# Performance work log

Hardware: AMD Instinct MI355X
Metric: run time of the kernel (lower is better)

Reference implementation:

```python
import jax, jax.numpy as jnp
import numpy as np

D_MODEL = 512
N = 2048
BS = 8


def setup_inputs() -> dict:
    key = jax.random.key(0)
    ks = jax.random.split(key, 5)
    inputs1 = jax.random.normal(ks[0], (BS, N, D_MODEL), dtype=jnp.float32)
    inputs2 = jax.random.normal(ks[1], (BS, N, D_MODEL), dtype=jnp.float32)
    # torch Linear weights: init.normal_(std=0.001), bias=0
    Wq = 0.001 * jax.random.normal(ks[2], (D_MODEL, D_MODEL), dtype=jnp.float32)
    Wk = 0.001 * jax.random.normal(ks[3], (D_MODEL, D_MODEL), dtype=jnp.float32)
    Wv = 0.001 * jax.random.normal(ks[4], (D_MODEL, D_MODEL), dtype=jnp.float32)
    bq = jnp.zeros((D_MODEL,), dtype=jnp.float32)
    bk = jnp.zeros((D_MODEL,), dtype=jnp.float32)
    bv = jnp.zeros((D_MODEL,), dtype=jnp.float32)
    # nn.Parameter(torch.ones((n, n)))
    position_biases = jnp.ones((N, N), dtype=jnp.float32)
    return {"inputs1": inputs1, "inputs2": inputs2, "Wq": Wq, "bq": bq,
            "Wk": Wk, "bk": bk, "Wv": Wv, "bv": bv,
            "position_biases": position_biases}


def reference(inputs1, inputs2, Wq, bq, Wk, bk, Wv, bv, position_biases):
    # torch Linear: y = x @ W.T + b
    q = inputs1 @ Wq.T + bq                     # [b, n, d]
    k = inputs1 @ Wk.T + bk                     # [b, s, d]
    v = inputs2 @ Wv.T + bv                     # [b, s, d]
    # exp(k[b,s,d] + bias[t,s]) = exp(bias)[t,s] * exp(k)[b,s,d] -> separable,
    # avoiding the original's (n, bs, n, dim) broadcast intermediate.
    expB = jnp.exp(position_biases)             # [t, s]
    ek = jnp.exp(k)                             # [b, s, d]
    num = jnp.einsum('ts,bsd->btd', expB, ek * v)
    den = jnp.einsum('ts,bsd->btd', expB, ek)
    return jax.nn.sigmoid(q) * (num / den)      # [b, n, d]
```

## Files before the change

kernel.cpp:

```cpp
#include <hip/hip_runtime.h>

typedef float  f32x4  __attribute__((ext_vector_type(4)));
typedef __bf16 bf16x8 __attribute__((ext_vector_type(8)));
typedef __bf16 bf16x4 __attribute__((ext_vector_type(4)));

#define D_MODEL 512
#define SEQ     2048
#define BATCH   8
#define ROWS    (BATCH * SEQ)

#define ASYNC_COPY16(dst_lds, src_glb)                                          \
  __builtin_amdgcn_global_load_lds(                                             \
      (const __attribute__((address_space(1))) void*)(src_glb),                 \
      (__attribute__((address_space(3))) void*)(dst_lds), 16, 0, 0)

__global__ void cvt_all_kernel(const float* __restrict__ x1,
                               const float* __restrict__ x2,
                               const float* __restrict__ posb,
                               const float* __restrict__ Wq,
                               const float* __restrict__ Wk,
                               const float* __restrict__ Wv,
                               __bf16* __restrict__ x1b, __bf16* __restrict__ x2b,
                               __bf16* __restrict__ expBb, __bf16* __restrict__ wb)
{
  const int blk = blockIdx.x;
  if (blk < 16384) {
    const float* in = (blk < 8192) ? x1 : x2;
    __bf16* out = (blk < 8192) ? x1b : x2b;
    const int i = (blk & 8191) * 256 + threadIdx.x;
    float4 v = ((const float4*)in)[i];
    bf16x4 o = { (__bf16)v.x, (__bf16)v.y, (__bf16)v.z, (__bf16)v.w };
    ((bf16x4*)out)[i] = o;
  } else if (blk < 20480) {
    const int i = (blk - 16384) * 256 + threadIdx.x;
    float4 v = ((const float4*)posb)[i];
    bf16x4 o = { (__bf16)__expf(v.x), (__bf16)__expf(v.y),
                 (__bf16)__expf(v.z), (__bf16)__expf(v.w) };
    ((bf16x4*)expBb)[i] = o;
  } else {
    const int i = (blk - 20480) * 256 + threadIdx.x;
    const int nW4 = D_MODEL * D_MODEL / 4;
    const float* src = (i < nW4) ? Wq : (i < 2 * nW4) ? Wk : Wv;
    const int ii = i - ((i < nW4) ? 0 : (i < 2 * nW4) ? nW4 : 2 * nW4);
    float4 v = ((const float4*)src)[ii];
    bf16x4 o = { (__bf16)v.x, (__bf16)v.y, (__bf16)v.z, (__bf16)v.w };
    ((bf16x4*)wb)[i] = o;
  }
}

__global__ __launch_bounds__(512) void q_gemm_kernel(
    const __bf16* __restrict__ x1b, const __bf16* __restrict__ wb,
    const float* __restrict__ bq, __bf16* __restrict__ sigq)
{
  extern __shared__ __align__(16) __bf16 smem[];

  const int K = D_MODEL;
  const int tid  = threadIdx.x;
  const int wave = tid >> 6;
  const int lane = tid & 63;
  const int quad = lane >> 4;
  const int l16  = lane & 15;
  const int wm   = (wave >> 1) * 64;
  const int wn   = (wave & 1) * 64;
  const int m0   = blockIdx.x * 256;
  const int n0   = blockIdx.y * 128;
  const int l8r  = lane >> 3;
  const int scol = ((lane & 7) ^ l8r) * 8;

  const __bf16* ga[4]; const __bf16* gb[2];
  #pragma unroll
  for (int i = 0; i < 4; ++i)
    ga[i] = x1b + (long long)(m0 + i * 64 + wave * 8 + l8r) * K + scol;
  #pragma unroll
  for (int i = 0; i < 2; ++i)
    gb[i] = wb + (long long)(n0 + i * 64 + wave * 8 + l8r) * K + scol;

  f32x4 acc[4][4];
  #pragma unroll
  for (int i = 0; i < 4; ++i)
    #pragma unroll
    for (int j = 0; j < 4; ++j) acc[i][j] = (f32x4){0.f, 0.f, 0.f, 0.f};

  auto stageA2 = [&](int c, int k0, int i0) {
    ASYNC_COPY16(smem + c * 16384 + (i0 * 64 + wave * 8) * 64, ga[i0] + k0);
    ASYNC_COPY16(smem + c * 16384 + ((i0 + 1) * 64 + wave * 8) * 64, ga[i0 + 1] + k0);
  };
  auto stageB1 = [&](int c, int k0, int i) {
    ASYNC_COPY16(smem + 32768 + c * 8192 + (i * 64 + wave * 8) * 64, gb[i] + k0);
  };

  stageA2(0, 0, 0); stageA2(0, 0, 2);
  stageB1(0, 0, 0); stageB1(0, 0, 1);

  const int s0 = ((quad    ) ^ (l16 & 7)) * 8;
  const int s1 = ((quad + 4) ^ (l16 & 7)) * 8;

  for (int t = 0; t < 8; ++t) {
    const int c = t & 1;
    asm volatile("s_waitcnt vmcnt(0)" ::: "memory");
    __builtin_amdgcn_s_barrier();
    __builtin_amdgcn_sched_barrier(0);

    const __bf16* Ac = smem +         c * 16384 + (wm + l16) * 64;
    const __bf16* Bc = smem + 32768 + c * 8192  + (wn + l16) * 64;
    const bool pf = (t + 1 < 8);
    const int k1 = (t + 1) * 64;

    bf16x8 bfr[4][2];
    #pragma unroll
    for (int p = 0; p < 2; ++p) {
      if (p == 0) {
        #pragma unroll
        for (int j = 0; j < 4; ++j) {
          bfr[j][0] = *(const bf16x8*)&Bc[j * 1024 + s0];
          bfr[j][1] = *(const bf16x8*)&Bc[j * 1024 + s1];
        }
      }
      bf16x8 af[2][2];
      #pragma unroll
      for (int ii = 0; ii < 2; ++ii) {
        af[ii][0] = *(const bf16x8*)&Ac[(p * 2 + ii) * 1024 + s0];
        af[ii][1] = *(const bf16x8*)&Ac[(p * 2 + ii) * 1024 + s1];
      }
      if (pf) {
        if (p == 0) { stageA2(c ^ 1, k1, 0); stageB1(c ^ 1, k1, 0); }
        else        { stageA2(c ^ 1, k1, 2); stageB1(c ^ 1, k1, 1); }
      }
      __builtin_amdgcn_s_barrier();
      asm volatile("s_waitcnt lgkmcnt(0)" ::: "memory");
      __builtin_amdgcn_sched_barrier(0);
      __builtin_amdgcn_s_setprio(1);
      #pragma unroll
      for (int kk = 0; kk < 2; ++kk)
        #pragma unroll
        for (int ii = 0; ii < 2; ++ii)
          #pragma unroll
          for (int j = 0; j < 4; ++j)
            acc[p * 2 + ii][j] = __builtin_amdgcn_mfma_f32_16x16x32_bf16(
                af[ii][kk], bfr[j][kk], acc[p * 2 + ii][j], 0, 0, 0);
      __builtin_amdgcn_s_setprio(0);
      __builtin_amdgcn_s_barrier();
    }
  }

  #pragma unroll
  for (int j = 0; j < 4; ++j) {
    const int col = n0 + wn + j * 16 + l16;
    const float bvv = bq[col];
    #pragma unroll
    for (int i = 0; i < 4; ++i) {
      #pragma unroll
      for (int r = 0; r < 4; ++r) {
        const int row = m0 + wm + i * 16 + quad * 4 + r;
        float x = acc[i][j][r] + bvv;
        sigq[(long long)row * D_MODEL + col] = (__bf16)(1.f / (1.f + __expf(-x)));
      }
    }
  }
}

__global__ __launch_bounds__(512) void kv_fused_kernel(
    const __bf16* __restrict__ x1b, const __bf16* __restrict__ x2b,
    const __bf16* __restrict__ wb,
    const float* __restrict__ bk, const float* __restrict__ bv,
    __bf16* __restrict__ ekvT)
{
  extern __shared__ __align__(16) __bf16 smem[];

  const int K = D_MODEL;
  const int tid  = threadIdx.x;
  const int wave = tid >> 6;
  const int lane = tid & 63;
  const int quad = lane >> 4;
  const int l16  = lane & 15;
  const int wm   = (wave >> 1) * 64;
  const int wn   = (wave & 1) * 64;
  const int F0   = blockIdx.y * 256;
  const int L0   = blockIdx.x * 128;
  const int l8r  = lane >> 3;
  const int scol = ((lane & 7) ^ l8r) * 8;

  const __bf16* Wkb = wb + (long long)D_MODEL * D_MODEL;
  const __bf16* Wvb = wb + 2LL * D_MODEL * D_MODEL;

  const __bf16* gWk[4]; const __bf16* gWv[4];
  const __bf16* gX1[2]; const __bf16* gX2[2];
  #pragma unroll
  for (int i = 0; i < 4; ++i) {
    gWk[i] = Wkb + (long long)(F0 + i * 64 + wave * 8 + l8r) * K + scol;
    gWv[i] = Wvb + (long long)(F0 + i * 64 + wave * 8 + l8r) * K + scol;
  }
  #pragma unroll
  for (int i = 0; i < 2; ++i) {
    gX1[i] = x1b + (long long)(L0 + i * 64 + wave * 8 + l8r) * K + scol;
    gX2[i] = x2b + (long long)(L0 + i * 64 + wave * 8 + l8r) * K + scol;
  }

  f32x4 acck[4][4], accv[4][4];
  #pragma unroll
  for (int i = 0; i < 4; ++i)
    #pragma unroll
    for (int j = 0; j < 4; ++j) {
      acck[i][j] = (f32x4){0.f, 0.f, 0.f, 0.f};
      accv[i][j] = (f32x4){0.f, 0.f, 0.f, 0.f};
    }

  auto stgW = [&](int c, int i, const __bf16* p) {
    ASYNC_COPY16(smem + c * 16384 + (i * 64 + wave * 8) * 64, p);
  };
  auto stgX = [&](int c, int i, const __bf16* p) {
    ASYNC_COPY16(smem + 32768 + c * 8192 + (i * 64 + wave * 8) * 64, p);
  };

  stgW(0, 0, gWk[0]); stgW(0, 1, gWk[1]); stgW(0, 2, gWk[2]); stgW(0, 3, gWk[3]);
  stgX(0, 0, gX1[0]); stgX(0, 1, gX1[1]);

  const int s0 = ((quad    ) ^ (l16 & 7)) * 8;
  const int s1 = ((quad + 4) ^ (l16 & 7)) * 8;

  auto pass = [&](f32x4 (&acc)[4][4], bool vpass) {
    for (int t = 0; t < 8; ++t) {
      const int c = t & 1;
      asm volatile("s_waitcnt vmcnt(0)" ::: "memory");
      __builtin_amdgcn_s_barrier();
      __builtin_amdgcn_sched_barrier(0);

      const __bf16* Ac = smem +         c * 16384 + (wm + l16) * 64;
      const __bf16* Bc = smem + 32768 + c * 8192  + (wn + l16) * 64;
      const bool nx = (t == 7);
      const bool pf = !(vpass && nx);
      const bool sv = vpass || nx;
      const int k1 = nx ? 0 : (t + 1) * 64;

      bf16x8 bfr[4][2];
      #pragma unroll
      for (int p = 0; p < 2; ++p) {
        if (p == 0) {
          #pragma unroll
          for (int j = 0; j < 4; ++j) {
            bfr[j][0] = *(const bf16x8*)&Bc[j * 1024 + s0];
            bfr[j][1] = *(const bf16x8*)&Bc[j * 1024 + s1];
          }
        }
        bf16x8 af[2][2];
        #pragma unroll
        for (int ii = 0; ii < 2; ++ii) {
          af[ii][0] = *(const bf16x8*)&Ac[(p * 2 + ii) * 1024 + s0];
          af[ii][1] = *(const bf16x8*)&Ac[(p * 2 + ii) * 1024 + s1];
        }
        if (pf) {
          if (p == 0) {
            stgW(c ^ 1, 0, (sv ? gWv[0] : gWk[0]) + k1);
            stgW(c ^ 1, 1, (sv ? gWv[1] : gWk[1]) + k1);
            stgX(c ^ 1, 0, (sv ? gX2[0] : gX1[0]) + k1);
          } else {
            stgW(c ^ 1, 2, (sv ? gWv[2] : gWk[2]) + k1);
            stgW(c ^ 1, 3, (sv ? gWv[3] : gWk[3]) + k1);
            stgX(c ^ 1, 1, (sv ? gX2[1] : gX1[1]) + k1);
          }
        }
        __builtin_amdgcn_s_barrier();
        asm volatile("s_waitcnt lgkmcnt(0)" ::: "memory");
        __builtin_amdgcn_sched_barrier(0);
        __builtin_amdgcn_s_setprio(1);
        #pragma unroll
        for (int kk = 0; kk < 2; ++kk)
          #pragma unroll
          for (int ii = 0; ii < 2; ++ii)
            #pragma unroll
            for (int j = 0; j < 4; ++j)
              acc[p * 2 + ii][j] = __builtin_amdgcn_mfma_f32_16x16x32_bf16(
                  af[ii][kk], bfr[j][kk], acc[p * 2 + ii][j], 0, 0, 0);
        __builtin_amdgcn_s_setprio(0);
        __builtin_amdgcn_s_barrier();
      }
    }
  };

  pass(acck, false);
  pass(accv, true);

  const int b   = L0 >> 11;
  const int sb  = L0 & 2047;
  __bf16* outb = ekvT + (long long)b * (2 * D_MODEL) * SEQ + sb;
  #pragma unroll
  for (int i = 0; i < 4; ++i) {
    #pragma unroll
    for (int r = 0; r < 4; ++r) {
      const int d = F0 + wm + i * 16 + quad * 4 + r;
      const float bkd = bk[d];
      const float bvd = bv[d];
      const int gr = ((d >> 5) << 6) + (d & 31);
      #pragma unroll
      for (int j = 0; j < 4; ++j) {
        const int ss = wn + j * 16 + l16;
        const float kkv = acck[i][j][r] + bkd;
        const float vvv = accv[i][j][r] + bvd;
        const float ekf = __expf(kkv);
        outb[(long long)gr * SEQ + ss]        = (__bf16)(ekf * vvv);
        outb[(long long)(gr + 32) * SEQ + ss] = (__bf16)ekf;
      }
    }
  }
}

#define EBM 256
#define EBN 256
#define EBK 64
#define ENT (SEQ / EBK)

__global__ __launch_bounds__(512) void einsum_fused_kernel(
    const __bf16* __restrict__ A, const __bf16* __restrict__ BtAll,
    const __bf16* __restrict__ sigq, float* __restrict__ out)
{
  extern __shared__ __align__(16) __bf16 smem[];

  const int b = blockIdx.z;
  const __bf16* Bt = BtAll + (long long)b * (2 * D_MODEL) * SEQ;

  const int tid  = threadIdx.x;
  const int wave = tid >> 6;
  const int lane = tid & 63;
  const int quad = lane >> 4;
  const int l16  = lane & 15;
  const int wm   = (wave >> 2) * 128;
  const int wn   = (wave & 3) * 64;
  const int m0   = blockIdx.x * EBM;
  const int n0   = blockIdx.y * EBN;
  const int l8r  = lane >> 3;
  const int scol = ((lane & 7) ^ l8r) * 8;

  const __bf16* gA = A  + (long long)(m0 + wave * 8 + l8r) * SEQ + scol;
  const __bf16* gB = Bt + (long long)(n0 + wave * 8 + l8r) * SEQ + scol;
  __bf16* lA = smem +         (wave * 8) * 64;
  __bf16* lB = smem + 32768 + (wave * 8) * 64;

  f32x4 acc[8][4];
  #pragma unroll
  for (int i = 0; i < 8; ++i)
    #pragma unroll
    for (int j = 0; j < 4; ++j) acc[i][j] = (f32x4){0.f, 0.f, 0.f, 0.f};

  auto stage_pair = [&](int c, int k0, int i) {
    ASYNC_COPY16(lA + c * 16384 + i * 4096, gA + (long long)i * 64 * SEQ + k0);
    ASYNC_COPY16(lB + c * 16384 + i * 4096, gB + (long long)i * 64 * SEQ + k0);
  };

  #pragma unroll
  for (int i = 0; i < 4; ++i) stage_pair(0, 0, i);

  const int s0 = ((quad    ) ^ (l16 & 7)) * 8;
  const int s1 = ((quad + 4) ^ (l16 & 7)) * 8;

  for (int t = 0; t < ENT; ++t) {
    const int c = t & 1;
    asm volatile("s_waitcnt vmcnt(0)" ::: "memory");
    __builtin_amdgcn_s_barrier();
    __builtin_amdgcn_sched_barrier(0);

    const __bf16* Ac = smem +         c * 16384 + (wm + l16) * 64;
    const __bf16* Bc = smem + 32768 + c * 16384 + (wn + l16) * 64;
    const bool pf = (t + 1 < ENT);
    const int k1 = (t + 1) * EBK;

    bf16x8 bfr[4][2];
    #pragma unroll
    for (int q = 0; q < 4; ++q) {
      if (q == 0) {
        #pragma unroll
        for (int j = 0; j < 4; ++j) {
          bfr[j][0] = *(const bf16x8*)&Bc[j * 1024 + s0];
          bfr[j][1] = *(const bf16x8*)&Bc[j * 1024 + s1];
        }
      }
      bf16x8 af[2][2];
      #pragma unroll
      for (int ii = 0; ii < 2; ++ii) {
        af[ii][0] = *(const bf16x8*)&Ac[(q * 2 + ii) * 1024 + s0];
        af[ii][1] = *(const bf16x8*)&Ac[(q * 2 + ii) * 1024 + s1];
      }
      if (pf) {
        if (q == 0) { stage_pair(c ^ 1, k1, 0); stage_pair(c ^ 1, k1, 1); }
        else if (q == 1) { stage_pair(c ^ 1, k1, 2); stage_pair(c ^ 1, k1, 3); }
      }
      __builtin_amdgcn_s_barrier();
      asm volatile("s_waitcnt lgkmcnt(0)" ::: "memory");
      __builtin_amdgcn_sched_barrier(0);
      __builtin_amdgcn_s_setprio(1);
      #pragma unroll
      for (int kk = 0; kk < 2; ++kk)
        #pragma unroll
        for (int ii = 0; ii < 2; ++ii)
          #pragma unroll
          for (int j = 0; j < 4; ++j)
            acc[q * 2 + ii][j] = __builtin_amdgcn_mfma_f32_16x16x32_bf16(
                af[ii][kk], bfr[j][kk], acc[q * 2 + ii][j], 0, 0, 0);
      __builtin_amdgcn_s_setprio(0);
      __builtin_amdgcn_s_barrier();
    }
  }

  const int g = (n0 + wn) >> 6;
  #pragma unroll
  for (int j = 0; j < 2; ++j) {
    const int d = g * 32 + j * 16 + l16;
    #pragma unroll
    for (int i = 0; i < 8; ++i) {
      #pragma unroll
      for (int r = 0; r < 4; ++r) {
        const int row = m0 + wm + i * 16 + quad * 4 + r;
        const long long off = ((long long)b * SEQ + row) * D_MODEL + d;
        const float num = acc[i][j][r];
        const float den = acc[i][j + 2][r];
        out[off] = (float)sigq[off] * (num / den);
      }
    }
  }
}

extern "C" void kernel_launch(void* const* d_in, const int* in_sizes, int n_in,
                              void* d_out, int out_size, void* d_ws, size_t ws_size,
                              hipStream_t stream) {
  const float* inputs1 = (const float*)d_in[0];
  const float* inputs2 = (const float*)d_in[1];
  const float* Wq = (const float*)d_in[2];
  const float* bq = (const float*)d_in[3];
  const float* Wk = (const float*)d_in[4];
  const float* bk = (const float*)d_in[5];
  const float* Wv = (const float*)d_in[6];
  const float* bv = (const float*)d_in[7];
  const float* posb = (const float*)d_in[8];
  float* out = (float*)d_out;

  char* ws = (char*)d_ws;
  const long long szX  = (long long)ROWS * D_MODEL * 2;
  const long long szW  = (long long)D_MODEL * D_MODEL * 2;
  const long long szEB = (long long)SEQ * SEQ * 2;
  const long long szT  = (long long)BATCH * 2 * D_MODEL * SEQ * 2;
  __bf16* x1b   = (__bf16*)(ws);                 ws += szX;
  __bf16* x2b   = (__bf16*)(ws);                 ws += szX;
  __bf16* wb    = (__bf16*)(ws);                 ws += 3 * szW;
  __bf16* expBb = (__bf16*)(ws);                 ws += szEB;
  __bf16* sigq  = (__bf16*)(ws);                 ws += szX;
  __bf16* ekvT  = (__bf16*)(ws);                 ws += szT;

  static bool attr_done = false;
  if (!attr_done) {
    hipFuncSetAttribute((const void*)einsum_fused_kernel,
                        hipFuncAttributeMaxDynamicSharedMemorySize, 131072);
    hipFuncSetAttribute((const void*)q_gemm_kernel,
                        hipFuncAttributeMaxDynamicSharedMemorySize, 98304);
    hipFuncSetAttribute((const void*)kv_fused_kernel,
                        hipFuncAttributeMaxDynamicSharedMemorySize, 98304);
    attr_done = true;
  }

  cvt_all_kernel<<<21248, 256, 0, stream>>>(inputs1, inputs2, posb,
                                            Wq, Wk, Wv,
                                            x1b, x2b, expBb, wb);

  {
    dim3 g(ROWS / 256, D_MODEL / 128);
    q_gemm_kernel<<<g, 512, 98304, stream>>>(x1b, wb, bq, sigq);
  }

  {
    dim3 g(ROWS / 128, D_MODEL / 256);
    kv_fused_kernel<<<g, 512, 98304, stream>>>(x1b, x2b, wb, bk, bv, ekvT);
  }

  {
    dim3 g(SEQ / EBM, (2 * D_MODEL) / EBN, BATCH);
    einsum_fused_kernel<<<g, 512, 131072, stream>>>(expBb, ekvT, sigq, out);
  }
}
```

Baseline: 239.5 us.

## Fuse fp32-to-bf16 activation conversion into GEMM loaders

Drops the separate pass that converted both activation tensors to bf16. The Q and KV GEMMs now load fp32 activations straight into registers, convert them, and write bf16 into LDS in the swizzled layout. This removes a full write and re-read of two 16 MB bf16 buffers plus the work of many conversion blocks. In exchange, the GEMMs read twice as many activation bytes, the x1 tile is read and converted by both GEMMs, and the async LDS copy becomes a register round-trip with an extra lgkmcnt wait before each barrier.

New measurement: 246.8 us. 3.1% more time.

```diff
diff --git a/kernel.cpp b/kernel.cpp
--- a/kernel.cpp
+++ b/kernel.cpp
@@ -14,31 +14,28 @@
       (const __attribute__((address_space(1))) void*)(src_glb),                 \
       (__attribute__((address_space(3))) void*)(dst_lds), 16, 0, 0)
 
-__global__ void cvt_all_kernel(const float* __restrict__ x1,
-                               const float* __restrict__ x2,
-                               const float* __restrict__ posb,
+__device__ __forceinline__ bf16x8 cvt_f32x8(float4 a, float4 b) {
+  bf16x8 o;
+  o[0] = (__bf16)a.x; o[1] = (__bf16)a.y; o[2] = (__bf16)a.z; o[3] = (__bf16)a.w;
+  o[4] = (__bf16)b.x; o[5] = (__bf16)b.y; o[6] = (__bf16)b.z; o[7] = (__bf16)b.w;
+  return o;
+}
+
+__global__ void cvt_all_kernel(const float* __restrict__ posb,
                                const float* __restrict__ Wq,
                                const float* __restrict__ Wk,
                                const float* __restrict__ Wv,
-                               __bf16* __restrict__ x1b, __bf16* __restrict__ x2b,
                                __bf16* __restrict__ expBb, __bf16* __restrict__ wb)
 {
   const int blk = blockIdx.x;
-  if (blk < 16384) {
-    const float* in = (blk < 8192) ? x1 : x2;
-    __bf16* out = (blk < 8192) ? x1b : x2b;
-    const int i = (blk & 8191) * 256 + threadIdx.x;
-    float4 v = ((const float4*)in)[i];
-    bf16x4 o = { (__bf16)v.x, (__bf16)v.y, (__bf16)v.z, (__bf16)v.w };
-    ((bf16x4*)out)[i] = o;
-  } else if (blk < 20480) {
-    const int i = (blk - 16384) * 256 + threadIdx.x;
+  if (blk < 4096) {
+    const int i = blk * 256 + threadIdx.x;
     float4 v = ((const float4*)posb)[i];
     bf16x4 o = { (__bf16)__expf(v.x), (__bf16)__expf(v.y),
                  (__bf16)__expf(v.z), (__bf16)__expf(v.w) };
     ((bf16x4*)expBb)[i] = o;
   } else {
-    const int i = (blk - 20480) * 256 + threadIdx.x;
+    const int i = (blk - 4096) * 256 + threadIdx.x;
     const int nW4 = D_MODEL * D_MODEL / 4;
     const float* src = (i < nW4) ? Wq : (i < 2 * nW4) ? Wk : Wv;
     const int ii = i - ((i < nW4) ? 0 : (i < 2 * nW4) ? nW4 : 2 * nW4);
@@ -49,7 +46,7 @@
 }
 
 __global__ __launch_bounds__(512) void q_gemm_kernel(
-    const __bf16* __restrict__ x1b, const __bf16* __restrict__ wb,
+    const float* __restrict__ x1f, const __bf16* __restrict__ wb,
     const float* __restrict__ bq, __bf16* __restrict__ sigq)
 {
   extern __shared__ __align__(16) __bf16 smem[];
@@ -67,10 +64,10 @@
   const int l8r  = lane >> 3;
   const int scol = ((lane & 7) ^ l8r) * 8;
 
-  const __bf16* ga[4]; const __bf16* gb[2];
+  const float* gaf[4]; const __bf16* gb[2];
   #pragma unroll
   for (int i = 0; i < 4; ++i)
-    ga[i] = x1b + (long long)(m0 + i * 64 + wave * 8 + l8r) * K + scol;
+    gaf[i] = x1f + (long long)(m0 + i * 64 + wave * 8 + l8r) * K + scol;
   #pragma unroll
   for (int i = 0; i < 2; ++i)
     gb[i] = wb + (long long)(n0 + i * 64 + wave * 8 + l8r) * K + scol;
@@ -81,15 +78,22 @@
     #pragma unroll
     for (int j = 0; j < 4; ++j) acc[i][j] = (f32x4){0.f, 0.f, 0.f, 0.f};
 
-  auto stageA2 = [&](int c, int k0, int i0) {
-    ASYNC_COPY16(smem + c * 16384 + (i0 * 64 + wave * 8) * 64, ga[i0] + k0);
-    ASYNC_COPY16(smem + c * 16384 + ((i0 + 1) * 64 + wave * 8) * 64, ga[i0 + 1] + k0);
+  float4 aA[4][2];
+  auto loadA = [&](int k0, int i) {
+    aA[i][0] = *(const float4*)(gaf[i] + k0);
+    aA[i][1] = *(const float4*)(gaf[i] + k0 + 4);
+  };
+  auto writeA = [&](int c) {
+    #pragma unroll
+    for (int i = 0; i < 4; ++i)
+      *(bf16x8*)(smem + c * 16384 + (i * 64 + wave * 8) * 64 + lane * 8) =
+          cvt_f32x8(aA[i][0], aA[i][1]);
   };
   auto stageB1 = [&](int c, int k0, int i) {
     ASYNC_COPY16(smem + 32768 + c * 8192 + (i * 64 + wave * 8) * 64, gb[i] + k0);
   };
 
-  stageA2(0, 0, 0); stageA2(0, 0, 2);
+  loadA(0, 0); loadA(0, 1); loadA(0, 2); loadA(0, 3);
   stageB1(0, 0, 0); stageB1(0, 0, 1);
 
   const int s0 = ((quad    ) ^ (l16 & 7)) * 8;
@@ -98,6 +102,8 @@
   for (int t = 0; t < 8; ++t) {
     const int c = t & 1;
     asm volatile("s_waitcnt vmcnt(0)" ::: "memory");
+    writeA(c);
+    asm volatile("s_waitcnt lgkmcnt(0)" ::: "memory");
     __builtin_amdgcn_s_barrier();
     __builtin_amdgcn_sched_barrier(0);
 
@@ -123,8 +129,8 @@
         af[ii][1] = *(const bf16x8*)&Ac[(p * 2 + ii) * 1024 + s1];
       }
       if (pf) {
-        if (p == 0) { stageA2(c ^ 1, k1, 0); stageB1(c ^ 1, k1, 0); }
-        else        { stageA2(c ^ 1, k1, 2); stageB1(c ^ 1, k1, 1); }
+        if (p == 0) { loadA(k1, 0); loadA(k1, 1); stageB1(c ^ 1, k1, 0); }
+        else        { loadA(k1, 2); loadA(k1, 3); stageB1(c ^ 1, k1, 1); }
       }
       __builtin_amdgcn_s_barrier();
       asm volatile("s_waitcnt lgkmcnt(0)" ::: "memory");
@@ -160,7 +166,7 @@
 }
 
 __global__ __launch_bounds__(512) void kv_fused_kernel(
-    const __bf16* __restrict__ x1b, const __bf16* __restrict__ x2b,
+    const float* __restrict__ x1f, const float* __restrict__ x2f,
     const __bf16* __restrict__ wb,
     const float* __restrict__ bk, const float* __restrict__ bv,
     __bf16* __restrict__ ekvT)
@@ -184,7 +190,7 @@
   const __bf16* Wvb = wb + 2LL * D_MODEL * D_MODEL;
 
   const __bf16* gWk[4]; const __bf16* gWv[4];
-  const __bf16* gX1[2]; const __bf16* gX2[2];
+  const float*  gX1[2]; const float*  gX2[2];
   #pragma unroll
   for (int i = 0; i < 4; ++i) {
     gWk[i] = Wkb + (long long)(F0 + i * 64 + wave * 8 + l8r) * K + scol;
@@ -192,8 +198,8 @@
   }
   #pragma unroll
   for (int i = 0; i < 2; ++i) {
-    gX1[i] = x1b + (long long)(L0 + i * 64 + wave * 8 + l8r) * K + scol;
-    gX2[i] = x2b + (long long)(L0 + i * 64 + wave * 8 + l8r) * K + scol;
+    gX1[i] = x1f + (long long)(L0 + i * 64 + wave * 8 + l8r) * K + scol;
+    gX2[i] = x2f + (long long)(L0 + i * 64 + wave * 8 + l8r) * K + scol;
   }
 
   f32x4 acck[4][4], accv[4][4];
@@ -205,15 +211,23 @@
       accv[i][j] = (f32x4){0.f, 0.f, 0.f, 0.f};
     }
 
+  float4 xr[2][2];
+  auto loadX = [&](const float* p, int i) {
+    xr[i][0] = *(const float4*)(p);
+    xr[i][1] = *(const float4*)(p + 4);
+  };
+  auto writeX = [&](int c) {
+    #pragma unroll
+    for (int i = 0; i < 2; ++i)
+      *(bf16x8*)(smem + 32768 + c * 8192 + (i * 64 + wave * 8) * 64 + lane * 8) =
+          cvt_f32x8(xr[i][0], xr[i][1]);
+  };
   auto stgW = [&](int c, int i, const __bf16* p) {
     ASYNC_COPY16(smem + c * 16384 + (i * 64 + wave * 8) * 64, p);
   };
-  auto stgX = [&](int c, int i, const __bf16* p) {
-    ASYNC_COPY16(smem + 32768 + c * 8192 + (i * 64 + wave * 8) * 64, p);
-  };
 
   stgW(0, 0, gWk[0]); stgW(0, 1, gWk[1]); stgW(0, 2, gWk[2]); stgW(0, 3, gWk[3]);
-  stgX(0, 0, gX1[0]); stgX(0, 1, gX1[1]);
+  loadX(gX1[0], 0); loadX(gX1[1], 1);
 
   const int s0 = ((quad    ) ^ (l16 & 7)) * 8;
   const int s1 = ((quad + 4) ^ (l16 & 7)) * 8;
@@ -222,6 +236,8 @@
     for (int t = 0; t < 8; ++t) {
       const int c = t & 1;
       asm volatile("s_waitcnt vmcnt(0)" ::: "memory");
+      writeX(c);
+      asm volatile("s_waitcnt lgkmcnt(0)" ::: "memory");
       __builtin_amdgcn_s_barrier();
       __builtin_amdgcn_sched_barrier(0);
 
@@ -252,11 +268,11 @@
           if (p == 0) {
             stgW(c ^ 1, 0, (sv ? gWv[0] : gWk[0]) + k1);
             stgW(c ^ 1, 1, (sv ? gWv[1] : gWk[1]) + k1);
-            stgX(c ^ 1, 0, (sv ? gX2[0] : gX1[0]) + k1);
+            loadX((sv ? gX2[0] : gX1[0]) + k1, 0);
           } else {
             stgW(c ^ 1, 2, (sv ? gWv[2] : gWk[2]) + k1);
             stgW(c ^ 1, 3, (sv ? gWv[3] : gWk[3]) + k1);
-            stgX(c ^ 1, 1, (sv ? gX2[1] : gX1[1]) + k1);
+            loadX((sv ? gX2[1] : gX1[1]) + k1, 1);
           }
         }
         __builtin_amdgcn_s_barrier();
@@ -437,8 +453,6 @@
   const long long szW  = (long long)D_MODEL * D_MODEL * 2;
   const long long szEB = (long long)SEQ * SEQ * 2;
   const long long szT  = (long long)BATCH * 2 * D_MODEL * SEQ * 2;
-  __bf16* x1b   = (__bf16*)(ws);                 ws += szX;
-  __bf16* x2b   = (__bf16*)(ws);                 ws += szX;
   __bf16* wb    = (__bf16*)(ws);                 ws += 3 * szW;
   __bf16* expBb = (__bf16*)(ws);                 ws += szEB;
   __bf16* sigq  = (__bf16*)(ws);                 ws += szX;
@@ -455,18 +469,16 @@
     attr_done = true;
   }
 
-  cvt_all_kernel<<<21248, 256, 0, stream>>>(inputs1, inputs2, posb,
-                                            Wq, Wk, Wv,
-                                            x1b, x2b, expBb, wb);
+  cvt_all_kernel<<<4864, 256, 0, stream>>>(posb, Wq, Wk, Wv, expBb, wb);
 
   {
     dim3 g(ROWS / 256, D_MODEL / 128);
-    q_gemm_kernel<<<g, 512, 98304, stream>>>(x1b, wb, bq, sigq);
+    q_gemm_kernel<<<g, 512, 98304, stream>>>(inputs1, wb, bq, sigq);
   }
 
   {
     dim3 g(ROWS / 128, D_MODEL / 256);
-    kv_fused_kernel<<<g, 512, 98304, stream>>>(x1b, x2b, wb, bk, bv, ekvT);
+    kv_fused_kernel<<<g, 512, 98304, stream>>>(inputs1, inputs2, wb, bk, bv, ekvT);
   }
 
   {
```

## Enlarge Q GEMM tile to 256x256 and use grid-stride 8-wide conversion kernel

Applied to the files above, without the earlier changes.

The Q projection GEMM tile grows from 256x128 to 256x256, so each wave computes a 128x64 sub-tile with twice the accumulators. This halves the number of blocks and reduces redundant reloads of x1 across the N dimension, at the cost of more registers and 128KB of LDS, which may lower occupancy. Separately, the conversion kernel becomes a grid-stride loop over 2048 blocks in which each thread converts 8 elements, aiming to cut launch and indexing overhead.

After: 253.8 us. +6.0%, slower.

```diff
diff --git a/kernel.cpp b/kernel.cpp
--- a/kernel.cpp
+++ b/kernel.cpp
@@ -14,37 +14,49 @@
       (const __attribute__((address_space(1))) void*)(src_glb),                 \
       (__attribute__((address_space(3))) void*)(dst_lds), 16, 0, 0)
 
-__global__ void cvt_all_kernel(const float* __restrict__ x1,
-                               const float* __restrict__ x2,
-                               const float* __restrict__ posb,
-                               const float* __restrict__ Wq,
-                               const float* __restrict__ Wk,
-                               const float* __restrict__ Wv,
-                               __bf16* __restrict__ x1b, __bf16* __restrict__ x2b,
-                               __bf16* __restrict__ expBb, __bf16* __restrict__ wb)
+__device__ __forceinline__ bf16x8 cvt8(float4 a, float4 b) {
+  bf16x8 o;
+  o[0] = (__bf16)a.x; o[1] = (__bf16)a.y; o[2] = (__bf16)a.z; o[3] = (__bf16)a.w;
+  o[4] = (__bf16)b.x; o[5] = (__bf16)b.y; o[6] = (__bf16)b.z; o[7] = (__bf16)b.w;
+  return o;
+}
+
+__global__ __launch_bounds__(256) void cvt_all_kernel(
+    const float* __restrict__ x1, const float* __restrict__ x2,
+    const float* __restrict__ posb,
+    const float* __restrict__ Wq, const float* __restrict__ Wk,
+    const float* __restrict__ Wv,
+    __bf16* __restrict__ x1b, __bf16* __restrict__ x2b,
+    __bf16* __restrict__ expBb, __bf16* __restrict__ wb)
 {
-  const int blk = blockIdx.x;
-  if (blk < 16384) {
-    const float* in = (blk < 8192) ? x1 : x2;
-    __bf16* out = (blk < 8192) ? x1b : x2b;
-    const int i = (blk & 8191) * 256 + threadIdx.x;
-    float4 v = ((const float4*)in)[i];
-    bf16x4 o = { (__bf16)v.x, (__bf16)v.y, (__bf16)v.z, (__bf16)v.w };
-    ((bf16x4*)out)[i] = o;
-  } else if (blk < 20480) {
-    const int i = (blk - 16384) * 256 + threadIdx.x;
-    float4 v = ((const float4*)posb)[i];
-    bf16x4 o = { (__bf16)__expf(v.x), (__bf16)__expf(v.y),
-                 (__bf16)__expf(v.z), (__bf16)__expf(v.w) };
-    ((bf16x4*)expBb)[i] = o;
-  } else {
-    const int i = (blk - 20480) * 256 + threadIdx.x;
-    const int nW4 = D_MODEL * D_MODEL / 4;
-    const float* src = (i < nW4) ? Wq : (i < 2 * nW4) ? Wk : Wv;
-    const int ii = i - ((i < nW4) ? 0 : (i < 2 * nW4) ? nW4 : 2 * nW4);
-    float4 v = ((const float4*)src)[ii];
-    bf16x4 o = { (__bf16)v.x, (__bf16)v.y, (__bf16)v.z, (__bf16)v.w };
-    ((bf16x4*)wb)[i] = o;
+  const long long total = 2719744LL;
+  for (long long c = (long long)blockIdx.x * 256 + threadIdx.x; c < total;
+       c += (long long)gridDim.x * 256) {
+    if (c < 2097152) {
+      const bool two = (c >= 1048576);
+      const long long off = (c - (two ? 1048576 : 0)) * 8;
+      const float* src = two ? x2 : x1;
+      __bf16* dst = two ? x2b : x1b;
+      float4 a = *(const float4*)(src + off);
+      float4 b = *(const float4*)(src + off + 4);
+      *(bf16x8*)(dst + off) = cvt8(a, b);
+    } else if (c < 2621440) {
+      const long long off = (c - 2097152) * 8;
+      float4 a = *(const float4*)(posb + off);
+      float4 b = *(const float4*)(posb + off + 4);
+      float4 ea = { __expf(a.x), __expf(a.y), __expf(a.z), __expf(a.w) };
+      float4 eb = { __expf(b.x), __expf(b.y), __expf(b.z), __expf(b.w) };
+      *(bf16x8*)(expBb + off) = cvt8(ea, eb);
+    } else {
+      const long long w = (c - 2621440) * 8;
+      const long long nW = (long long)D_MODEL * D_MODEL;
+      const int sel = (int)(w / nW);
+      const float* src = (sel == 0) ? Wq : (sel == 1) ? Wk : Wv;
+      const long long so = w - (long long)sel * nW;
+      float4 a = *(const float4*)(src + so);
+      float4 b = *(const float4*)(src + so + 4);
+      *(bf16x8*)(wb + w) = cvt8(a, b);
+    }
   }
 }
 
@@ -60,37 +72,31 @@
   const int lane = tid & 63;
   const int quad = lane >> 4;
   const int l16  = lane & 15;
-  const int wm   = (wave >> 1) * 64;
-  const int wn   = (wave & 1) * 64;
+  const int wm   = (wave >> 2) * 128;
+  const int wn   = (wave & 3) * 64;
   const int m0   = blockIdx.x * 256;
-  const int n0   = blockIdx.y * 128;
+  const int n0   = blockIdx.y * 256;
   const int l8r  = lane >> 3;
   const int scol = ((lane & 7) ^ l8r) * 8;
 
-  const __bf16* ga[4]; const __bf16* gb[2];
-  #pragma unroll
-  for (int i = 0; i < 4; ++i)
-    ga[i] = x1b + (long long)(m0 + i * 64 + wave * 8 + l8r) * K + scol;
-  #pragma unroll
-  for (int i = 0; i < 2; ++i)
-    gb[i] = wb + (long long)(n0 + i * 64 + wave * 8 + l8r) * K + scol;
-
-  f32x4 acc[4][4];
-  #pragma unroll
-  for (int i = 0; i < 4; ++i)
+  const __bf16* gA = x1b + (long long)(m0 + wave * 8 + l8r) * K + scol;
+  const __bf16* gB = wb  + (long long)(n0 + wave * 8 + l8r) * K + scol;
+  __bf16* lA = smem +         (wave * 8) * 64;
+  __bf16* lB = smem + 32768 + (wave * 8) * 64;
+
+  f32x4 acc[8][4];
+  #pragma unroll
+  for (int i = 0; i < 8; ++i)
     #pragma unroll
     for (int j = 0; j < 4; ++j) acc[i][j] = (f32x4){0.f, 0.f, 0.f, 0.f};
 
-  auto stageA2 = [&](int c, int k0, int i0) {
-    ASYNC_COPY16(smem + c * 16384 + (i0 * 64 + wave * 8) * 64, ga[i0] + k0);
-    ASYNC_COPY16(smem + c * 16384 + ((i0 + 1) * 64 + wave * 8) * 64, ga[i0 + 1] + k0);
+  auto stage_pair = [&](int c, int k0, int i) {
+    ASYNC_COPY16(lA + c * 16384 + i * 4096, gA + (long long)i * 64 * K + k0);
+    ASYNC_COPY16(lB + c * 16384 + i * 4096, gB + (long long)i * 64 * K + k0);
   };
-  auto stageB1 = [&](int c, int k0, int i) {
-    ASYNC_COPY16(smem + 32768 + c * 8192 + (i * 64 + wave * 8) * 64, gb[i] + k0);
-  };
-
-  stageA2(0, 0, 0); stageA2(0, 0, 2);
-  stageB1(0, 0, 0); stageB1(0, 0, 1);
+
+  #pragma unroll
+  for (int i = 0; i < 4; ++i) stage_pair(0, 0, i);
 
   const int s0 = ((quad    ) ^ (l16 & 7)) * 8;
   const int s1 = ((quad + 4) ^ (l16 & 7)) * 8;
@@ -102,14 +108,14 @@
     __builtin_amdgcn_sched_barrier(0);
 
     const __bf16* Ac = smem +         c * 16384 + (wm + l16) * 64;
-    const __bf16* Bc = smem + 32768 + c * 8192  + (wn + l16) * 64;
+    const __bf16* Bc = smem + 32768 + c * 16384 + (wn + l16) * 64;
     const bool pf = (t + 1 < 8);
     const int k1 = (t + 1) * 64;
 
     bf16x8 bfr[4][2];
     #pragma unroll
-    for (int p = 0; p < 2; ++p) {
-      if (p == 0) {
+    for (int q = 0; q < 4; ++q) {
+      if (q == 0) {
         #pragma unroll
         for (int j = 0; j < 4; ++j) {
           bfr[j][0] = *(const bf16x8*)&Bc[j * 1024 + s0];
@@ -119,12 +125,12 @@
       bf16x8 af[2][2];
       #pragma unroll
       for (int ii = 0; ii < 2; ++ii) {
-        af[ii][0] = *(const bf16x8*)&Ac[(p * 2 + ii) * 1024 + s0];
-        af[ii][1] = *(const bf16x8*)&Ac[(p * 2 + ii) * 1024 + s1];
+        af[ii][0] = *(const bf16x8*)&Ac[(q * 2 + ii) * 1024 + s0];
+        af[ii][1] = *(const bf16x8*)&Ac[(q * 2 + ii) * 1024 + s1];
       }
       if (pf) {
-        if (p == 0) { stageA2(c ^ 1, k1, 0); stageB1(c ^ 1, k1, 0); }
-        else        { stageA2(c ^ 1, k1, 2); stageB1(c ^ 1, k1, 1); }
+        if (q == 0) { stage_pair(c ^ 1, k1, 0); stage_pair(c ^ 1, k1, 1); }
+        else if (q == 1) { stage_pair(c ^ 1, k1, 2); stage_pair(c ^ 1, k1, 3); }
       }
       __builtin_amdgcn_s_barrier();
       asm volatile("s_waitcnt lgkmcnt(0)" ::: "memory");
@@ -136,8 +142,8 @@
         for (int ii = 0; ii < 2; ++ii)
           #pragma unroll
           for (int j = 0; j < 4; ++j)
-            acc[p * 2 + ii][j] = __builtin_amdgcn_mfma_f32_16x16x32_bf16(
-                af[ii][kk], bfr[j][kk], acc[p * 2 + ii][j], 0, 0, 0);
+            acc[q * 2 + ii][j] = __builtin_amdgcn_mfma_f32_16x16x32_bf16(
+                af[ii][kk], bfr[j][kk], acc[q * 2 + ii][j], 0, 0, 0);
       __builtin_amdgcn_s_setprio(0);
       __builtin_amdgcn_s_barrier();
     }
@@ -148,7 +154,7 @@
     const int col = n0 + wn + j * 16 + l16;
     const float bvv = bq[col];
     #pragma unroll
-    for (int i = 0; i < 4; ++i) {
+    for (int i = 0; i < 8; ++i) {
       #pragma unroll
       for (int r = 0; r < 4; ++r) {
         const int row = m0 + wm + i * 16 + quad * 4 + r;
@@ -449,19 +455,19 @@
     hipFuncSetAttribute((const void*)einsum_fused_kernel,
                         hipFuncAttributeMaxDynamicSharedMemorySize, 131072);
     hipFuncSetAttribute((const void*)q_gemm_kernel,
-                        hipFuncAttributeMaxDynamicSharedMemorySize, 98304);
+                        hipFuncAttributeMaxDynamicSharedMemorySize, 131072);
     hipFuncSetAttribute((const void*)kv_fused_kernel,
                         hipFuncAttributeMaxDynamicSharedMemorySize, 98304);
     attr_done = true;
   }
 
-  cvt_all_kernel<<<21248, 256, 0, stream>>>(inputs1, inputs2, posb,
-                                            Wq, Wk, Wv,
-                                            x1b, x2b, expBb, wb);
+  cvt_all_kernel<<<2048, 256, 0, stream>>>(inputs1, inputs2, posb,
+                                           Wq, Wk, Wv,
+                                           x1b, x2b, expBb, wb);
 
   {
-    dim3 g(ROWS / 256, D_MODEL / 128);
-    q_gemm_kernel<<<g, 512, 98304, stream>>>(x1b, wb, bq, sigq);
+    dim3 g(ROWS / 256, D_MODEL / 256);
+    q_gemm_kernel<<<g, 512, 131072, stream>>>(x1b, wb, bq, sigq);
   }
 
   {
```
